# Kernel tuning notes

Hardware: AMD Instinct MI355X
Metric: run time of the kernel (lower is better)

Reference implementation:

```python
import jax, jax.numpy as jnp
import numpy as np

# MoE config (mirrors init_kwargs)
E = 8        # num_experts
K = 2        # num_experts_per_tok
H = 1024     # hidden_size
F = 2816     # moe_intermediate_size
B, S = 2, 512
NORM_TOPK = True


def setup_inputs() -> dict:
    key = jax.random.key(0)
    ks = jax.random.split(key, 5)
    x = jax.random.normal(ks[0], (B, S, H), dtype=jnp.float32)
    router_w = jax.random.normal(ks[1], (E, H), dtype=jnp.float32) * 0.02   # nn.Linear(H, E).weight
    gate_proj = jax.random.normal(ks[2], (E, H, F), dtype=jnp.float32) * 0.02
    up_proj = jax.random.normal(ks[3], (E, H, F), dtype=jnp.float32) * 0.02
    down_proj = jax.random.normal(ks[4], (E, F, H), dtype=jnp.float32) * 0.02
    return {"x": x, "router_w": router_w, "gate_proj": gate_proj,
            "up_proj": up_proj, "down_proj": down_proj}


def reference(x, router_w, gate_proj, up_proj, down_proj):
    b, s, h = x.shape
    xf = x.reshape(-1, h)                                    # [T, H]
    # Router: softmax over experts, top-k selection mask
    logits = xf @ router_w.T                                 # [T, E]
    probs = jax.nn.softmax(logits, axis=-1)
    topk_p, topk_i = jax.lax.top_k(probs, K)                 # [T, K]
    routing_map = jax.nn.one_hot(topk_i, E, dtype=probs.dtype).sum(axis=1)  # [T, E] 0/1
    if NORM_TOPK:
        probs = probs / topk_p.sum(-1, keepdims=True)
    weight = probs * routing_map                             # [T, E]; zero for unselected experts
    # Per-expert SwiGLU FFN; combine weighted by routing prob.
    # Dense-masked formulation: mathematically identical to the original
    # gather -> per-expert GEMM -> scatter_add, since weight==0 for unrouted pairs.
    g = jnp.einsum('th,ehf->tef', xf, gate_proj)             # [T, E, F]
    u = jnp.einsum('th,ehf->tef', xf, up_proj)               # [T, E, F]
    m = jax.nn.silu(g) * u                                   # [T, E, F]
    out = jnp.einsum('tef,efh,te->th', m, down_proj, weight) # [T, H]
    return out.reshape(b, s, h)
```

## Files before the change

kernel.cpp:

```cpp
#include <hip/hip_runtime.h>

#define HD 1024
#define FD 2816
#define NE 8
#define NT 1024
#define NSLOT (NT * 2)

typedef short short8 __attribute__((ext_vector_type(8)));
typedef unsigned u32x4 __attribute__((ext_vector_type(4)));
typedef unsigned u32x2 __attribute__((ext_vector_type(2)));
typedef float f32x4 __attribute__((ext_vector_type(4)));
typedef float f32x16 __attribute__((ext_vector_type(16)));

typedef __attribute__((address_space(3))) unsigned lds_u32;
typedef __attribute__((address_space(1))) const unsigned glb_u32;

#define WAITV(N) asm volatile("s_waitcnt vmcnt(" #N ") lgkmcnt(0)" ::: "memory")
#define BARRIER() do { __builtin_amdgcn_s_barrier(); __builtin_amdgcn_sched_barrier(0); } while (0)
#define SB() __builtin_amdgcn_sched_barrier(0)

__device__ __forceinline__ void glds16(const void* g, void* l) {
  __builtin_amdgcn_global_load_lds((glb_u32*)g, (lds_u32*)l, 16, 0, 0);
}

__device__ __forceinline__ short f2bf(float f) {
  unsigned u = __builtin_bit_cast(unsigned, f);
  u += 0x7FFFu + ((u >> 16) & 1u);
  return (short)(u >> 16);
}
__device__ __forceinline__ unsigned cvtpk(float lo, float hi) {
  unsigned r;
  asm("v_cvt_pk_bf16_f32 %0, %1, %2" : "=v"(r) : "v"(lo), "v"(hi));
  return r;
}
__device__ __forceinline__ int imin(int a, int b) { return a < b ? a : b; }

__global__ void router_kernel(const float* __restrict__ x,
                              const float* __restrict__ rw,
                              int* __restrict__ counts,
                              int* __restrict__ tok_i,
                              float* __restrict__ tok_w) {
  const int t = blockIdx.x;
  const int lane = threadIdx.x;
  const float* px = x + (size_t)t * HD;
  float acc[NE];
#pragma unroll
  for (int e = 0; e < NE; e++) acc[e] = 0.f;
  for (int h = lane; h < HD; h += 64) {
    float xv = px[h];
#pragma unroll
    for (int e = 0; e < NE; e++) acc[e] += xv * rw[e * HD + h];
  }
#pragma unroll
  for (int e = 0; e < NE; e++) {
#pragma unroll
    for (int off = 32; off > 0; off >>= 1)
      acc[e] += __shfl_xor(acc[e], off, 64);
  }
  if (lane == 0) {
    float mx = acc[0];
#pragma unroll
    for (int e = 1; e < NE; e++) mx = fmaxf(mx, acc[e]);
    float ex[NE];
#pragma unroll
    for (int e = 0; e < NE; e++) ex[e] = __expf(acc[e] - mx);
    int i1 = 0;
#pragma unroll
    for (int e = 1; e < NE; e++) if (ex[e] > ex[i1]) i1 = e;
    int i2 = (i1 == 0) ? 1 : 0;
#pragma unroll
    for (int e = 0; e < NE; e++) if (e != i1 && ex[e] > ex[i2]) i2 = e;
    float inv = 1.f / (ex[i1] + ex[i2]);
    tok_i[t * 2 + 0] = i1; tok_w[t * 2 + 0] = ex[i1] * inv;
    tok_i[t * 2 + 1] = i2; tok_w[t * 2 + 1] = ex[i2] * inv;
    atomicAdd(&counts[i1], 1);
    atomicAdd(&counts[i2], 1);
  }
}

__global__ void scanfill_kernel(const int* __restrict__ counts,
                                const int* __restrict__ tok_i,
                                const float* __restrict__ tok_w,
                                int* __restrict__ bases,
                                int* __restrict__ slot_token,
                                float* __restrict__ slot_w) {
  __shared__ int cur[NE];
  const int t = threadIdx.x;
  if (t == 0) {
    int s = 0;
    for (int e = 0; e < NE; e++) { bases[e] = s; cur[e] = s; s += counts[e]; }
    bases[NE] = s;
  }
  __syncthreads();
#pragma unroll
  for (int k = 0; k < 2; k++) {
    int e = tok_i[t * 2 + k];
    int pos = atomicAdd(&cur[e], 1);
    slot_token[pos] = t;
    slot_w[pos] = tok_w[t * 2 + k];
  }
}

__device__ __forceinline__ void pack_block(const float* __restrict__ W,
                                           short* __restrict__ P, int K, int N,
                                           int f0, int kt, int e, int tid,
                                           char* smem) {
  const int KT = K >> 5;
  const int lane = tid & 63, w = tid >> 6;
  const float* src = W + (size_t)e * K * N + (size_t)(kt * 32 + w * 8) * N +
                     f0 + lane * 4;
  f32x4 x0 = *(const f32x4*)(src);
  f32x4 x1 = *(const f32x4*)(src + (size_t)N);
  f32x4 x2 = *(const f32x4*)(src + (size_t)2 * N);
  f32x4 x3 = *(const f32x4*)(src + (size_t)3 * N);
  f32x4 x4 = *(const f32x4*)(src + (size_t)4 * N);
  f32x4 x5 = *(const f32x4*)(src + (size_t)5 * N);
  f32x4 x6 = *(const f32x4*)(src + (size_t)6 * N);
  f32x4 x7 = *(const f32x4*)(src + (size_t)7 * N);
  unsigned* Lb = (unsigned*)(smem + w * 4608);
#pragma unroll
  for (int j = 0; j < 4; j++) {
    u32x4 c;
    c[0] = cvtpk(x0[j], x1[j]);
    c[1] = cvtpk(x2[j], x3[j]);
    c[2] = cvtpk(x4[j], x5[j]);
    c[3] = cvtpk(x6[j], x7[j]);
    int ch = 4 * lane + j;
    *(u32x4*)(Lb + (ch + (ch >> 3)) * 4) = c;
  }
  asm volatile("s_waitcnt lgkmcnt(0)" ::: "memory");
  SB();
  short* dstb = P + (((size_t)(e * KT + kt) * 4 + w) * N + f0) * 8;
#pragma unroll
  for (int j = 0; j < 4; j++) {
    int ch = j * 64 + lane;
    u32x4 c = *(const u32x4*)(Lb + (ch + (ch >> 3)) * 4);
    *(u32x4*)(dstb + (size_t)ch * 8) = c;
  }
}

__global__ __launch_bounds__(256, 4) void aux_kernel(
    const float* __restrict__ gw, const float* __restrict__ uw,
    const float* __restrict__ dwv, short* __restrict__ Pg,
    short* __restrict__ Pu, short* __restrict__ Pd,
    const float* __restrict__ x, const int* __restrict__ slot_token,
    short* __restrict__ xg, int pguN, int pdN) {
  __shared__ char smem[18432];
  const int bid = blockIdx.x;
  const int tid = threadIdx.x;
  if (bid < pguN) {
    const int f0 = (bid % 11) * 256;
    const int kt = (bid / 11) % 32;
    const int ez = bid / 352;
    pack_block(ez < NE ? gw : uw, ez < NE ? Pg : Pu, HD, FD, f0, kt, ez & 7,
               tid, smem);
  } else if (bid < pguN + pdN) {
    const int pid = bid - pguN;
    const int f0 = (pid & 3) * 256;
    const int kt = (pid >> 2) % 88;
    const int e = pid / 352;
    pack_block(dwv, Pd, FD, HD, f0, kt, e, tid, smem);
  } else {
    const int slot = bid - pguN - pdN;
    const int tok = slot_token[slot];
    f32x4 v = *(const f32x4*)(x + (size_t)tok * HD + tid * 4);
    u32x2 s;
    s[0] = cvtpk(v[0], v[1]);
    s[1] = cvtpk(v[2], v[3]);
    *(u32x2*)&xg[(size_t)slot * HD + tid * 4] = s;
  }
}


#define G_STAGE(S, T) do {                                           \
    glds16(asrc0 + (T) * 32, &As[S][wid * 512]);                     \
    glds16(asrc1 + (T) * 32, &As[S][2048 + wid * 512]);              \
    glds16(bgsrc + (size_t)(T) * 90112, &Bg[S][wid * 512]);          \
    glds16(busrc + (size_t)(T) * 90112, &Bu[S][wid * 512]);          \
  } while (0)

#define G_COMPUTE(S) do {                                                     \
    _Pragma("unroll")                                                         \
    for (int ks = 0; ks < 2; ks++) {                                          \
      const int oct = ks * 2 + l5;                                            \
      short8 a0, a1, bg, bu;                                                  \
      { int r = wm * 64 + l31, p = r >> 1;                                    \
        a0 = *(const short8*)&As[S][p * 64 +                                  \
              ((((r & 1) << 2) | oct) ^ (p & 7)) * 8]; }                      \
      { int r = wm * 64 + 32 + l31, p = r >> 1;                               \
        a1 = *(const short8*)&As[S][p * 64 +                                  \
              ((((r & 1) << 2) | oct) ^ (p & 7)) * 8]; }                      \
      { int n = wn * 32 + l31, pn = n >> 1;                                   \
        int off = pn * 64 + ((((n & 1) << 2) | oct) ^ (pn & 7)) * 8;          \
        bg = *(const short8*)&Bg[S][off];                                     \
        bu = *(const short8*)&Bu[S][off]; }                                   \
      accG0 = __builtin_amdgcn_mfma_f32_32x32x16_bf16(a0, bg, accG0, 0, 0, 0);\
      accU0 = __builtin_amdgcn_mfma_f32_32x32x16_bf16(a0, bu, accU0, 0, 0, 0);\
      accG1 = __builtin_amdgcn_mfma_f32_32x32x16_bf16(a1, bg, accG1, 0, 0, 0);\
      accU1 = __builtin_amdgcn_mfma_f32_32x32x16_bf16(a1, bu, accU1, 0, 0, 0);\
    }                                                                         \
  } while (0)

#define G_ITER(S, T) do {    \
    G_COMPUTE(S);            \
    BARRIER();               \
    G_STAGE(S, (T) + 3);     \
    WAITV(8);                \
    BARRIER();               \
  } while (0)

__global__ __launch_bounds__(256, 3) void gemm_gu_kernel(
    const short* __restrict__ xg, const short* __restrict__ Pg,
    const short* __restrict__ Pu, const int* __restrict__ bases,
    short* __restrict__ m_out) {
  const int bid = blockIdx.x;
  const int tid = threadIdx.x;
  const int gx = bid % 352;
  const int e = gx / 44, nt = gx - e * 44;
  const int b0 = bases[e];
  const int ne = bases[e + 1] - b0;
  const int row0 = (bid / 352) * 128;
  if (row0 >= ne) return;
  const int n0 = nt * 64;

  __shared__ short As[3][4096];
  __shared__ short Bg[3][2048];
  __shared__ short Bu[3][2048];

  const int lane = tid & 63, wid = tid >> 6;
  const int l31 = lane & 31, l5 = lane >> 5;
  const int wm = wid >> 1, wn = wid & 1;

  const short *asrc0, *asrc1;
  {
    int i = tid;
    int p = i >> 3, j = i & 7, v = j ^ (p & 7);
    int r = 2 * p + (v >> 2), c = v & 3;
    asrc0 = xg + (size_t)(b0 + imin(row0 + r, ne - 1)) * HD + c * 8;
    i = 256 + tid;
    p = i >> 3; j = i & 7; v = j ^ (p & 7);
    r = 2 * p + (v >> 2); c = v & 3;
    asrc1 = xg + (size_t)(b0 + imin(row0 + r, ne - 1)) * HD + c * 8;
  }
  const short *bgsrc, *busrc;
  {
    int p = tid >> 3, j = tid & 7, v = j ^ (p & 7);
    int r = 2 * p + (v >> 2), c = v & 3;
    size_t off = ((size_t)(e * 32 * 4 + c)) * (FD * 8) + (size_t)(n0 + r) * 8;
    bgsrc = Pg + off;
    busrc = Pu + off;
  }

  f32x16 accG0 = (f32x16)0.f, accG1 = (f32x16)0.f;
  f32x16 accU0 = (f32x16)0.f, accU1 = (f32x16)0.f;

  G_STAGE(0, 0); G_STAGE(1, 1); G_STAGE(2, 2);
  WAITV(8);
  BARRIER();

  for (int t = 0; t < 27; t += 3) {
    G_ITER(0, t);
    G_ITER(1, t + 1);
    G_ITER(2, t + 2);
  }
  G_ITER(0, 27);
  G_ITER(1, 28);
  G_COMPUTE(2);
  WAITV(4); BARRIER();
  G_COMPUTE(0);
  WAITV(0); BARRIER();
  G_COMPUTE(1);

#pragma unroll
  for (int q = 0; q < 16; q++) {
    int rb_ = (q & 3) + 8 * (q >> 2) + 4 * l5;
    {
      int r = row0 + wm * 64 + rb_;
      if (r < ne) {
        float g = accG0[q], u = accU0[q];
        float mv = (g / (1.f + __expf(-g))) * u;
        m_out[(size_t)(b0 + r) * FD + n0 + wn * 32 + l31] = f2bf(mv);
      }
    }
    {
      int r = row0 + wm * 64 + 32 + rb_;
      if (r < ne) {
        float g = accG1[q], u = accU1[q];
        float mv = (g / (1.f + __expf(-g))) * u;
        m_out[(size_t)(b0 + r) * FD + n0 + wn * 32 + l31] = f2bf(mv);
      }
    }
  }
}


#define D_STAGE(S, T) do {                                           \
    glds16(asrcA[0] + (T) * 64, &As[S][wid * 512]);                  \
    glds16(asrcA[1] + (T) * 64, &As[S][2048 + wid * 512]);           \
    glds16(asrcA[2] + (T) * 64, &As[S][4096 + wid * 512]);           \
    glds16(asrcA[3] + (T) * 64, &As[S][6144 + wid * 512]);           \
    glds16(bsrc0 + (size_t)(T) * 65536, &Bs[S][wid * 512]);          \
    glds16(bsrc1 + (size_t)(T) * 65536, &Bs[S][2048 + wid * 512]);   \
  } while (0)

#define D_COMPUTE(S) do {                                                     \
    _Pragma("unroll")                                                         \
    for (int ks = 0; ks < 4; ks++) {                                          \
      const int sub = ks >> 1, oct = (ks & 1) * 2 + l5;                       \
      short8 a0, a1, b;                                                       \
      { int r = wm * 64 + l31, p = r >> 1;                                    \
        a0 = *(const short8*)&As[S][sub * 4096 + p * 64 +                     \
              ((((r & 1) << 2) | oct) ^ (p & 7)) * 8]; }                      \
      { int r = wm * 64 + 32 + l31, p = r >> 1;                               \
        a1 = *(const short8*)&As[S][sub * 4096 + p * 64 +                     \
              ((((r & 1) << 2) | oct) ^ (p & 7)) * 8]; }                      \
      { int n = wn * 32 + l31, pn = n >> 1;                                   \
        b = *(const short8*)&Bs[S][sub * 2048 + pn * 64 +                     \
              ((((n & 1) << 2) | oct) ^ (pn & 7)) * 8]; }                     \
      acc0 = __builtin_amdgcn_mfma_f32_32x32x16_bf16(a0, b, acc0, 0, 0, 0);   \
      acc1 = __builtin_amdgcn_mfma_f32_32x32x16_bf16(a1, b, acc1, 0, 0, 0);   \
    }                                                                         \
  } while (0)

#define D_ITER(S, T) do {    \
    D_COMPUTE(S);            \
    BARRIER();               \
    D_STAGE(S, (T) + 3);     \
    WAITV(12);               \
    BARRIER();               \
  } while (0)

__global__ __launch_bounds__(256, 2) void down_kernel(
    const short* __restrict__ m_in, const short* __restrict__ Pd,
    const int* __restrict__ bases, const float* __restrict__ slot_w,
    const int* __restrict__ slot_token, float* __restrict__ out) {
  const int bx = blockIdx.x;
  const int e = bx >> 4, nt = bx & 15;
  const int b0 = bases[e];
  const int ne = bases[e + 1] - b0;
  const int row0 = blockIdx.y * 128;
  if (row0 >= ne) return;
  const int n0 = nt * 64;

  __shared__ short As[3][8192];
  __shared__ short Bs[3][4096];

  const int tid = threadIdx.x;
  const int lane = tid & 63, wid = tid >> 6;
  const int l31 = lane & 31, l5 = lane >> 5;
  const int wm = wid >> 1, wn = wid & 1;

  const short* asrcA[4];
#pragma unroll
  for (int q = 0; q < 4; q++) {
    int i = q * 256 + tid;
    int sub = i >> 9, ci = i & 511;
    int p = ci >> 3, j = ci & 7, v = j ^ (p & 7);
    int r = 2 * p + (v >> 2), c = v & 3;
    asrcA[q] = m_in + (size_t)(b0 + imin(row0 + r, ne - 1)) * FD + sub * 32 +
               c * 8;
  }
  const short *bsrc0, *bsrc1;
  {
    int p = tid >> 3, j = tid & 7, v = j ^ (p & 7);
    int r = 2 * p + (v >> 2), c = v & 3;
    bsrc0 = Pd + ((size_t)((e * 88 + 0) * 4 + c)) * (HD * 8) + (size_t)(n0 + r) * 8;
    bsrc1 = Pd + ((size_t)((e * 88 + 1) * 4 + c)) * (HD * 8) + (size_t)(n0 + r) * 8;
  }

  f32x16 acc0 = (f32x16)0.f, acc1 = (f32x16)0.f;

  D_STAGE(0, 0); D_STAGE(1, 1); D_STAGE(2, 2);
  WAITV(12);
  BARRIER();

  for (int t = 0; t < 39; t += 3) {
    D_ITER(0, t);
    D_ITER(1, t + 1);
    D_ITER(2, t + 2);
  }
  D_ITER(0, 39);
  D_ITER(1, 40);
  D_COMPUTE(2);
  WAITV(6); BARRIER();
  D_COMPUTE(0);
  WAITV(0); BARRIER();
  D_COMPUTE(1);

#pragma unroll
  for (int q = 0; q < 16; q++) {
    int rb_ = (q & 3) + 8 * (q >> 2) + 4 * l5;
    {
      int r = row0 + wm * 64 + rb_;
      if (r < ne) {
        int slot = b0 + r;
        atomicAdd(&out[(size_t)slot_token[slot] * HD + n0 + wn * 32 + l31],
                  acc0[q] * slot_w[slot]);
      }
    }
    {
      int r = row0 + wm * 64 + 32 + rb_;
      if (r < ne) {
        int slot = b0 + r;
        atomicAdd(&out[(size_t)slot_token[slot] * HD + n0 + wn * 32 + l31],
                  acc1[q] * slot_w[slot]);
      }
    }
  }
}

extern "C" void kernel_launch(void* const* d_in, const int* in_sizes, int n_in,
                              void* d_out, int out_size, void* d_ws,
                              size_t ws_size, hipStream_t stream) {
  const float* x = (const float*)d_in[0];
  const float* rw = (const float*)d_in[1];
  const float* gw = (const float*)d_in[2];
  const float* uw = (const float*)d_in[3];
  const float* dw = (const float*)d_in[4];
  float* out = (float*)d_out;

  char* ws = (char*)d_ws;
  int* counts = (int*)(ws + 0);
  int* bases = (int*)(ws + 128);
  int* tok_i = (int*)(ws + 256);
  float* tok_w = (float*)(ws + 8448);
  int* slot_token = (int*)(ws + 16640);
  float* slot_w = (float*)(ws + 24832);
  short* xg = (short*)(ws + 41216);
  short* m  = (short*)(ws + 4235520);
  short* Pg = (short*)(ws + 15769856);
  short* Pu = (short*)(ws + 61907200);
  short* PdBig = (short*)(ws + 108044544);
  const bool big = ws_size >= (size_t)108044544 + 46137344;
  short* Pd = big ? PdBig : Pg;

  (void)hipMemsetAsync(counts, 0, 64, stream);
  (void)hipMemsetAsync(out, 0, (size_t)out_size * 4, stream);
  router_kernel<<<NT, 64, 0, stream>>>(x, rw, counts, tok_i, tok_w);
  scanfill_kernel<<<1, 1024, 0, stream>>>(counts, tok_i, tok_w, bases,
                                          slot_token, slot_w);
  if (big) {
    aux_kernel<<<5632 + 2816 + 2048, 256, 0, stream>>>(
        gw, uw, dw, Pg, Pu, Pd, x, slot_token, xg, 5632, 2816);
    gemm_gu_kernel<<<352 * 8, 256, 0, stream>>>(xg, Pg, Pu, bases, m);
  } else {
    aux_kernel<<<5632 + 2048, 256, 0, stream>>>(
        gw, uw, dw, Pg, Pu, Pd, x, slot_token, xg, 5632, 0);
    gemm_gu_kernel<<<352 * 8, 256, 0, stream>>>(xg, Pg, Pu, bases, m);
    aux_kernel<<<2816, 256, 0, stream>>>(gw, uw, dw, Pg, Pu, Pd, x,
                                         slot_token, xg, 0, 2816);
  }
  down_kernel<<<dim3(128, 8), 256, 0, stream>>>(m, Pd, bases, slot_w,
                                                slot_token, out);
}
```

Baseline: 235.9 us.

## Move down-proj weight packing into gate/up GEMM launch and batch pack blocks

Down-projection weight packing moves out of the first auxiliary kernel and into extra leading blocks of the gate/up GEMM kernel. This lets packing of Pd overlap with the GEMM work instead of running before it, shortening the critical path ahead of the GEMM. Each pack and gather block now handles four work items, cutting the block count. The GEMM kernel's shared memory becomes a single byte array that both paths reuse, which may affect occupancy and scheduling. In the small-workspace path the GEMM-only and pack-only launches are kept separate.

```diff
diff --git a/kernel.cpp b/kernel.cpp
--- a/kernel.cpp
+++ b/kernel.cpp
@@ -139,35 +139,36 @@
   }
 }
 
-__global__ __launch_bounds__(256, 4) void aux_kernel(
+__global__ __launch_bounds__(256, 4) void pack_gu_gather_kernel(
     const float* __restrict__ gw, const float* __restrict__ uw,
-    const float* __restrict__ dwv, short* __restrict__ Pg,
-    short* __restrict__ Pu, short* __restrict__ Pd,
+    short* __restrict__ Pg, short* __restrict__ Pu,
     const float* __restrict__ x, const int* __restrict__ slot_token,
-    short* __restrict__ xg, int pguN, int pdN) {
+    short* __restrict__ xg) {
   __shared__ char smem[18432];
   const int bid = blockIdx.x;
   const int tid = threadIdx.x;
-  if (bid < pguN) {
-    const int f0 = (bid % 11) * 256;
-    const int kt = (bid / 11) % 32;
-    const int ez = bid / 352;
-    pack_block(ez < NE ? gw : uw, ez < NE ? Pg : Pu, HD, FD, f0, kt, ez & 7,
-               tid, smem);
-  } else if (bid < pguN + pdN) {
-    const int pid = bid - pguN;
-    const int f0 = (pid & 3) * 256;
-    const int kt = (pid >> 2) % 88;
-    const int e = pid / 352;
-    pack_block(dwv, Pd, FD, HD, f0, kt, e, tid, smem);
+  if (bid < 1408) {
+#pragma unroll
+    for (int i = 0; i < 4; i++) {
+      const int q = bid + i * 1408;
+      const int f0 = (q % 11) * 256;
+      const int kt = (q / 11) % 32;
+      const int ez = q / 352;
+      pack_block(ez < NE ? gw : uw, ez < NE ? Pg : Pu, HD, FD, f0, kt, ez & 7,
+                 tid, smem);
+    }
   } else {
-    const int slot = bid - pguN - pdN;
-    const int tok = slot_token[slot];
-    f32x4 v = *(const f32x4*)(x + (size_t)tok * HD + tid * 4);
-    u32x2 s;
-    s[0] = cvtpk(v[0], v[1]);
-    s[1] = cvtpk(v[2], v[3]);
-    *(u32x2*)&xg[(size_t)slot * HD + tid * 4] = s;
+    const int b = bid - 1408;
+#pragma unroll
+    for (int i = 0; i < 4; i++) {
+      const int slot = b + i * 512;
+      const int tok = slot_token[slot];
+      f32x4 v = *(const f32x4*)(x + (size_t)tok * HD + tid * 4);
+      u32x2 s;
+      s[0] = cvtpk(v[0], v[1]);
+      s[1] = cvtpk(v[2], v[3]);
+      *(u32x2*)&xg[(size_t)slot * HD + tid * 4] = s;
+    }
   }
 }
 
@@ -209,23 +210,39 @@
     BARRIER();               \
   } while (0)
 
-__global__ __launch_bounds__(256, 3) void gemm_gu_kernel(
+__global__ __launch_bounds__(256, 3) void gemm_gu_packd_kernel(
     const short* __restrict__ xg, const short* __restrict__ Pg,
     const short* __restrict__ Pu, const int* __restrict__ bases,
-    short* __restrict__ m_out) {
+    short* __restrict__ m_out, const float* __restrict__ dwv,
+    short* __restrict__ Pd, int packdB) {
+  __shared__ char smem[49152];
   const int bid = blockIdx.x;
   const int tid = threadIdx.x;
-  const int gx = bid % 352;
+
+  if (bid < packdB) {
+#pragma unroll
+    for (int i = 0; i < 4; i++) {
+      const int q = bid + i * 704;
+      const int f0 = (q & 3) * 256;
+      const int kt = (q >> 2) % 88;
+      const int e = q / 352;
+      pack_block(dwv, Pd, FD, HD, f0, kt, e, tid, smem);
+    }
+    return;
+  }
+
+  const int gbid = bid - packdB;
+  const int gx = gbid % 352;
   const int e = gx / 44, nt = gx - e * 44;
   const int b0 = bases[e];
   const int ne = bases[e + 1] - b0;
-  const int row0 = (bid / 352) * 128;
+  const int row0 = (gbid / 352) * 128;
   if (row0 >= ne) return;
   const int n0 = nt * 64;
 
-  __shared__ short As[3][4096];
-  __shared__ short Bg[3][2048];
-  __shared__ short Bu[3][2048];
+  short (*As)[4096] = (short(*)[4096])smem;
+  short (*Bg)[2048] = (short(*)[2048])(smem + 24576);
+  short (*Bu)[2048] = (short(*)[2048])(smem + 36864);
 
   const int lane = tid & 63, wid = tid >> 6;
   const int l31 = lane & 31, l5 = lane >> 5;
@@ -439,16 +456,16 @@
   router_kernel<<<NT, 64, 0, stream>>>(x, rw, counts, tok_i, tok_w);
   scanfill_kernel<<<1, 1024, 0, stream>>>(counts, tok_i, tok_w, bases,
                                           slot_token, slot_w);
+  pack_gu_gather_kernel<<<1408 + 512, 256, 0, stream>>>(gw, uw, Pg, Pu, x,
+                                                        slot_token, xg);
   if (big) {
-    aux_kernel<<<5632 + 2816 + 2048, 256, 0, stream>>>(
-        gw, uw, dw, Pg, Pu, Pd, x, slot_token, xg, 5632, 2816);
-    gemm_gu_kernel<<<352 * 8, 256, 0, stream>>>(xg, Pg, Pu, bases, m);
+    gemm_gu_packd_kernel<<<704 + 352 * 8, 256, 0, stream>>>(
+        xg, Pg, Pu, bases, m, dw, Pd, 704);
   } else {
-    aux_kernel<<<5632 + 2048, 256, 0, stream>>>(
-        gw, uw, dw, Pg, Pu, Pd, x, slot_token, xg, 5632, 0);
-    gemm_gu_kernel<<<352 * 8, 256, 0, stream>>>(xg, Pg, Pu, bases, m);
-    aux_kernel<<<2816, 256, 0, stream>>>(gw, uw, dw, Pg, Pu, Pd, x,
-                                         slot_token, xg, 0, 2816);
+    gemm_gu_packd_kernel<<<352 * 8, 256, 0, stream>>>(xg, Pg, Pu, bases, m,
+                                                      dw, Pd, 0);
+    gemm_gu_packd_kernel<<<704, 256, 0, stream>>>(xg, Pg, Pu, bases, m, dw,
+                                                  Pd, 704);
   }
   down_kernel<<<dim3(128, 8), 256, 0, stream>>>(m, Pd, bases, slot_w,
                                                 slot_token, out);
```

Result: faster. 221.7 us (-6.0%).

## Move down-proj weight packing into the gate/up GEMM launch as extra blocks

Applied to the files above, without the earlier changes.

The bf16 packing of the down-projection weights moves out of the auxiliary pre-GEMM kernel. It now runs as trailing blocks of the gate/up GEMM launch, so that conversion overlaps with GEMM work instead of delaying the GEMM start. The GEMM's LDS arrays are carved from a shared raw buffer so pack blocks and GEMM blocks can use the same shared memory. The GEMM grid also doubles its row tiles, adding blocks that exit early. Pack blocks may compete with GEMM blocks for bandwidth and CU slots.

```diff
diff --git a/kernel.cpp b/kernel.cpp
--- a/kernel.cpp
+++ b/kernel.cpp
@@ -139,29 +139,22 @@
   }
 }
 
-__global__ __launch_bounds__(256, 4) void aux_kernel(
+__global__ __launch_bounds__(256, 4) void pack_gu_gather_kernel(
     const float* __restrict__ gw, const float* __restrict__ uw,
-    const float* __restrict__ dwv, short* __restrict__ Pg,
-    short* __restrict__ Pu, short* __restrict__ Pd,
+    short* __restrict__ Pg, short* __restrict__ Pu,
     const float* __restrict__ x, const int* __restrict__ slot_token,
-    short* __restrict__ xg, int pguN, int pdN) {
+    short* __restrict__ xg) {
   __shared__ char smem[18432];
   const int bid = blockIdx.x;
   const int tid = threadIdx.x;
-  if (bid < pguN) {
+  if (bid < 5632) {
     const int f0 = (bid % 11) * 256;
     const int kt = (bid / 11) % 32;
     const int ez = bid / 352;
     pack_block(ez < NE ? gw : uw, ez < NE ? Pg : Pu, HD, FD, f0, kt, ez & 7,
                tid, smem);
-  } else if (bid < pguN + pdN) {
-    const int pid = bid - pguN;
-    const int f0 = (pid & 3) * 256;
-    const int kt = (pid >> 2) % 88;
-    const int e = pid / 352;
-    pack_block(dwv, Pd, FD, HD, f0, kt, e, tid, smem);
   } else {
-    const int slot = bid - pguN - pdN;
+    const int slot = bid - 5632;
     const int tok = slot_token[slot];
     f32x4 v = *(const f32x4*)(x + (size_t)tok * HD + tid * 4);
     u32x2 s;
@@ -209,12 +202,24 @@
     BARRIER();               \
   } while (0)
 
-__global__ __launch_bounds__(256, 3) void gemm_gu_kernel(
+__global__ __launch_bounds__(256, 3) void gemm_gu_packd_kernel(
     const short* __restrict__ xg, const short* __restrict__ Pg,
     const short* __restrict__ Pu, const int* __restrict__ bases,
-    short* __restrict__ m_out) {
+    short* __restrict__ m_out, const float* __restrict__ dwv,
+    short* __restrict__ Pd, int gemmN) {
+  __shared__ char smem[49152];
   const int bid = blockIdx.x;
   const int tid = threadIdx.x;
+
+  if (bid >= gemmN) {
+    const int pid = bid - gemmN;
+    const int f0 = (pid & 3) * 256;
+    const int kt = (pid >> 2) % 88;
+    const int e = pid / 352;
+    pack_block(dwv, Pd, FD, HD, f0, kt, e, tid, smem);
+    return;
+  }
+
   const int gx = bid % 352;
   const int e = gx / 44, nt = gx - e * 44;
   const int b0 = bases[e];
@@ -223,9 +228,9 @@
   if (row0 >= ne) return;
   const int n0 = nt * 64;
 
-  __shared__ short As[3][4096];
-  __shared__ short Bg[3][2048];
-  __shared__ short Bu[3][2048];
+  short (*As)[4096] = (short(*)[4096])smem;
+  short (*Bg)[2048] = (short(*)[2048])(smem + 24576);
+  short (*Bu)[2048] = (short(*)[2048])(smem + 36864);
 
   const int lane = tid & 63, wid = tid >> 6;
   const int l31 = lane & 31, l5 = lane >> 5;
@@ -439,16 +444,16 @@
   router_kernel<<<NT, 64, 0, stream>>>(x, rw, counts, tok_i, tok_w);
   scanfill_kernel<<<1, 1024, 0, stream>>>(counts, tok_i, tok_w, bases,
                                           slot_token, slot_w);
+  pack_gu_gather_kernel<<<7680, 256, 0, stream>>>(gw, uw, Pg, Pu, x,
+                                                  slot_token, xg);
   if (big) {
-    aux_kernel<<<5632 + 2816 + 2048, 256, 0, stream>>>(
-        gw, uw, dw, Pg, Pu, Pd, x, slot_token, xg, 5632, 2816);
-    gemm_gu_kernel<<<352 * 8, 256, 0, stream>>>(xg, Pg, Pu, bases, m);
+    gemm_gu_packd_kernel<<<5632 + 2816, 256, 0, stream>>>(
+        xg, Pg, Pu, bases, m, dw, Pd, 5632);
   } else {
-    aux_kernel<<<5632 + 2048, 256, 0, stream>>>(
-        gw, uw, dw, Pg, Pu, Pd, x, slot_token, xg, 5632, 0);
-    gemm_gu_kernel<<<352 * 8, 256, 0, stream>>>(xg, Pg, Pu, bases, m);
-    aux_kernel<<<2816, 256, 0, stream>>>(gw, uw, dw, Pg, Pu, Pd, x,
-                                         slot_token, xg, 0, 2816);
+    gemm_gu_packd_kernel<<<5632, 256, 0, stream>>>(xg, Pg, Pu, bases, m, dw,
+                                                   Pd, 5632);
+    gemm_gu_packd_kernel<<<2816, 256, 0, stream>>>(xg, Pg, Pu, bases, m, dw,
+                                                   Pd, 0);
   }
   down_kernel<<<dim3(128, 8), 256, 0, stream>>>(m, Pd, bases, slot_w,
                                                 slot_token, out);
```

Result: faster. 204.6 us (-13.3%).
